# Kernel tuning notes

Measured on AMD Instinct MI355X. Metric: run time of the kernel, lower is better.

The kernel has to match this reference:

```python
import jax, jax.numpy as jnp
import numpy as np

N_NODES = 50000
N_EDGES = 800000
D_IN, D1, D2, D_OUT = 128, 150, 100, 64


def setup_inputs() -> dict:
    key = jax.random.key(0)
    ks = jax.random.split(key, 10)
    x = jax.random.normal(ks[0], (N_NODES, D_IN), dtype=jnp.float32)
    src = jax.random.randint(ks[1], (N_EDGES,), 0, N_NODES, dtype=jnp.int32)
    dst = jax.random.randint(ks[2], (N_EDGES,), 0, N_NODES, dtype=jnp.int32)
    s1 = 1.0 / np.sqrt(D_IN)
    s2 = 1.0 / np.sqrt(D1)
    s3 = 1.0 / np.sqrt(D2)
    W1 = jax.random.uniform(ks[3], (D_IN, D1), jnp.float32, -s1, s1)
    b1 = jnp.zeros((D1,), jnp.float32)
    Wn = jax.random.uniform(ks[4], (D1, D2), jnp.float32, -s2, s2)
    Ws = jax.random.uniform(ks[5], (D1, D2), jnp.float32, -s2, s2)
    b2 = jnp.zeros((D2,), jnp.float32)
    W3 = jax.random.uniform(ks[6], (D2, D_OUT), jnp.float32, -s3, s3)
    b3 = jnp.zeros((D_OUT,), jnp.float32)
    return {"x": x, "src": src, "dst": dst, "W1": W1, "b1": b1,
            "Wn": Wn, "Ws": Ws, "b2": b2, "W3": W3, "b3": b3}


def _degrees(src, dst, n):
    ones = jnp.ones(src.shape[0], jnp.float32)
    deg_out = jax.ops.segment_sum(ones, src, num_segments=n)
    deg_in = jax.ops.segment_sum(ones, dst, num_segments=n)
    return deg_out, deg_in


def reference(x, src, dst, W1, b1, Wn, Ws, b2, W3, b3):
    n = x.shape[0]
    deg_out, deg_in = _degrees(src, dst, n)
    norm_out = jax.lax.rsqrt(jnp.maximum(deg_out, 1.0))  # [N]
    norm_in = jax.lax.rsqrt(jnp.maximum(deg_in, 1.0))    # [N]

    # --- GraphConv (norm='both'): D_in^{-1/2} A D_out^{-1/2} X W + b ---
    h = x * norm_out[:, None]                                   # [N, D_IN]
    agg = jax.ops.segment_sum(h[src], dst, num_segments=n)      # [N, D_IN]
    h = (agg * norm_in[:, None]) @ W1 + b1                      # [N, D1]
    h = jax.nn.elu(h)

    # --- SAGEConv (mean): fc_self(h) + fc_neigh(mean_neighbors(h)) + b ---
    neigh_sum = jax.ops.segment_sum(h[src], dst, num_segments=n)  # [N, D1]
    neigh = neigh_sum / jnp.maximum(deg_in, 1.0)[:, None]
    h = h @ Ws + neigh @ Wn + b2                                  # [N, D2]
    h = jax.nn.elu(h)

    # --- Dense + ELU ---
    out = jax.nn.elu(h @ W3 + b3)                                 # [N, D_OUT]
    return out
```

## Files before the change

kernel.cpp:

```cpp
#include <hip/hip_runtime.h>
#include <math.h>

#define N_NODES 50000
#define N_EDGES 800000
#define D_IN 128
#define D1 150
#define LD1 152
#define D2 100
#define LDP 100
#define D_OUT 64
#define SLOT 64
#define HBLK 64
#define HBIN 12500

#define LDS_K 40

using short8 = __attribute__((ext_vector_type(8))) short;
using f32x4  = __attribute__((ext_vector_type(4))) float;

__device__ __forceinline__ float elu(float v) { return v > 0.0f ? v : expm1f(v); }

__device__ __forceinline__ void split_bf16(float a, unsigned short& h, unsigned short& l) {
    unsigned int bits = __float_as_uint(a);
    unsigned int hb = (bits + 0x8000u) >> 16;
    h = (unsigned short)hb;
    float r = a - __uint_as_float(hb << 16);
    l = (unsigned short)((__float_as_uint(r) + 0x8000u) >> 16);
}

__device__ __forceinline__ void split8(const float4 a, const float4 b, short8& h, short8& l) {
    float f[8] = {a.x, a.y, a.z, a.w, b.x, b.y, b.z, b.w};
#pragma unroll
    for (int i = 0; i < 8; ++i) {
        unsigned short hh, ll;
        split_bf16(f[i], hh, ll);
        h[i] = (short)hh; l[i] = (short)ll;
    }
}

__device__ __forceinline__ float4 g_load4(const float* p) { return *(const float4*)p; }

__device__ __forceinline__ float4 g_load4_guard(const float* row, int kbase, int Klim, bool rowok) {
    float4 v;
    v.x = (rowok && kbase + 0 < Klim) ? row[kbase + 0] : 0.0f;
    v.y = (rowok && kbase + 1 < Klim) ? row[kbase + 1] : 0.0f;
    v.z = (rowok && kbase + 2 < Klim) ? row[kbase + 2] : 0.0f;
    v.w = (rowok && kbase + 3 < Klim) ? row[kbase + 3] : 0.0f;
    return v;
}

__device__ __forceinline__ void barrier_lgkm() {
    asm volatile("s_waitcnt lgkmcnt(0)\n\ts_barrier" ::: "memory");
    __builtin_amdgcn_sched_barrier(0);
}

__global__ __launch_bounds__(256) void hist_kernel(const int* __restrict__ src,
                                                   unsigned int* __restrict__ partial) {
    __shared__ unsigned int bins[HBIN];
    int tid = threadIdx.x, b = blockIdx.x;
    for (int i = tid; i < HBIN; i += 256) bins[i] = 0u;
    __syncthreads();
    int e0 = b * (N_EDGES / HBLK);
    int e1 = e0 + (N_EDGES / HBLK);
    for (int e = e0 + tid; e < e1; e += 256) {
        int s = src[e];
        atomicAdd(&bins[s >> 2], 1u << ((s & 3) * 8));
    }
    __syncthreads();
    unsigned int* outp = partial + (size_t)b * HBIN;
    for (int i = tid; i < HBIN; i += 256) outp[i] = bins[i];
}

__global__ __launch_bounds__(256) void norm_kernel(const unsigned int* __restrict__ partial,
                                                   float* __restrict__ norm_out) {
    int i = blockIdx.x * blockDim.x + threadIdx.x;
    if (i >= HBIN) return;
    unsigned int acc = 0;
#pragma unroll
    for (int h = 0; h < HBLK; ++h) acc += partial[(size_t)h * HBIN + i];
#pragma unroll
    for (int j = 0; j < 4; ++j) {
        unsigned int dg = (acc >> (j * 8)) & 0xFF;
        norm_out[i * 4 + j] = rsqrtf(fmaxf((float)dg, 1.0f));
    }
}

__global__ void fill_kernel(const int* __restrict__ src, const int* __restrict__ dst,
                            int* __restrict__ cursor, unsigned short* __restrict__ slots) {
    int e = blockIdx.x * blockDim.x + threadIdx.x;
    if (e < N_EDGES) {
        int d = dst[e], s = src[e];
        int pos = atomicAdd(&cursor[d], 1);
        if (pos < SLOT) slots[d * SLOT + pos] = (unsigned short)s;
    }
}

__global__ __launch_bounds__(256) void gather_x(const float* __restrict__ x,
                                                const float* __restrict__ norm_out,
                                                const int* __restrict__ deg_in,
                                                const unsigned short* __restrict__ slots,
                                                float* __restrict__ agg) {
    int wave = threadIdx.x >> 6;
    int lane = threadIdx.x & 63;
    int half = lane >> 5;
    int c = lane & 31;
    int n = blockIdx.x * 4 + wave;
    if (n >= N_NODES) return;
    int beg = n * SLOT;
    int dg = deg_in[n]; if (dg > SLOT) dg = SLOT;
    int end = beg + dg;
    float4 acc = {0.0f, 0.0f, 0.0f, 0.0f};
    int e = beg + half;
    for (; e + 6 < end; e += 8) {
        int s0 = slots[e];
        int s1 = slots[e + 2];
        int s2 = slots[e + 4];
        int s3 = slots[e + 6];
        float w0 = norm_out[s0], w1 = norm_out[s1];
        float w2 = norm_out[s2], w3 = norm_out[s3];
        float4 v0 = ((const float4*)(x + (size_t)s0 * D_IN))[c];
        float4 v1 = ((const float4*)(x + (size_t)s1 * D_IN))[c];
        float4 v2 = ((const float4*)(x + (size_t)s2 * D_IN))[c];
        float4 v3 = ((const float4*)(x + (size_t)s3 * D_IN))[c];
        acc.x += v0.x * w0 + v1.x * w1 + v2.x * w2 + v3.x * w3;
        acc.y += v0.y * w0 + v1.y * w1 + v2.y * w2 + v3.y * w3;
        acc.z += v0.z * w0 + v1.z * w1 + v2.z * w2 + v3.z * w3;
        acc.w += v0.w * w0 + v1.w * w1 + v2.w * w2 + v3.w * w3;
    }
    for (; e < end; e += 2) {
        int s = slots[e];
        float w = norm_out[s];
        float4 v = ((const float4*)(x + (size_t)s * D_IN))[c];
        acc.x += v.x * w; acc.y += v.y * w; acc.z += v.z * w; acc.w += v.w * w;
    }
    acc.x += __shfl_xor(acc.x, 32);
    acc.y += __shfl_xor(acc.y, 32);
    acc.z += __shfl_xor(acc.z, 32);
    acc.w += __shfl_xor(acc.w, 32);
    if (half == 0) ((float4*)(agg + (size_t)n * D_IN))[c] = acc;
}

__global__ __launch_bounds__(256) void gather_p(const float* __restrict__ p,
                                                const int* __restrict__ deg_in,
                                                const unsigned short* __restrict__ slots,
                                                float* __restrict__ ns) {
    int wave = threadIdx.x >> 6;
    int lane = threadIdx.x & 63;
    int half = lane >> 5;
    int c = lane & 31;
    bool cv = c < D2 / 4;
    int n = blockIdx.x * 4 + wave;
    if (n >= N_NODES) return;
    int beg = n * SLOT;
    int dg = deg_in[n]; if (dg > SLOT) dg = SLOT;
    int end = beg + dg;
    float4 acc = {0.0f, 0.0f, 0.0f, 0.0f};
    if (cv) {
        int e = beg + half;
        for (; e + 6 < end; e += 8) {
            int s0 = slots[e];
            int s1 = slots[e + 2];
            int s2 = slots[e + 4];
            int s3 = slots[e + 6];
            float4 v0 = ((const float4*)(p + (size_t)s0 * LDP))[c];
            float4 v1 = ((const float4*)(p + (size_t)s1 * LDP))[c];
            float4 v2 = ((const float4*)(p + (size_t)s2 * LDP))[c];
            float4 v3 = ((const float4*)(p + (size_t)s3 * LDP))[c];
            acc.x += (v0.x + v1.x) + (v2.x + v3.x);
            acc.y += (v0.y + v1.y) + (v2.y + v3.y);
            acc.z += (v0.z + v1.z) + (v2.z + v3.z);
            acc.w += (v0.w + v1.w) + (v2.w + v3.w);
        }
        for (; e < end; e += 2) {
            int s = slots[e];
            float4 v = ((const float4*)(p + (size_t)s * LDP))[c];
            acc.x += v.x; acc.y += v.y; acc.z += v.z; acc.w += v.w;
        }
    }
    acc.x += __shfl_xor(acc.x, 32);
    acc.y += __shfl_xor(acc.y, 32);
    acc.z += __shfl_xor(acc.z, 32);
    acc.w += __shfl_xor(acc.w, 32);
    if (half == 0 && cv) ((float4*)(ns + (size_t)n * LDP))[c] = acc;
}

template <int K, int KP, int NW, int LDA, int PRE, int EPI, int LDC, int GROUP>
__global__ __launch_bounds__(256, 5)
void gemm_mfma(const float* __restrict__ A, const float* __restrict__ W,
               const float* __restrict__ nsrc, const int* __restrict__ deg,
               const float* __restrict__ bstage, const float* __restrict__ bepi,
               float* __restrict__ C) {
    constexpr int NSTEP = KP / 32;
    constexpr int MBLK = (N_NODES + 63) / 64;
    __shared__ __align__(16) unsigned short AsH[64][LDS_K];
    __shared__ __align__(16) unsigned short AsL[64][LDS_K];
    __shared__ __align__(16) unsigned short BsH[64][LDS_K];
    __shared__ __align__(16) unsigned short BsL[64][LDS_K];

    const int b = blockIdx.x;
    const int cxcd = b & 7;
    const int sIdx = b >> 3;
    const int jj = sIdx / GROUP;
    const int yy = sIdx - jj * GROUP;
    const int xb = cxcd + 8 * jj;
    if (xb >= MBLK) return;
    const int m0 = xb * 64;
    const int n0 = yy * 64;

    const int tid = threadIdx.x;
    const int arow = tid >> 2;
    const int ak = (tid & 3) * 8;
    const int grow = m0 + arow;
    const bool rowok = grow < N_NODES;
    const int bn = tid & 63;
    const int bkg = tid >> 6;
    const int bcol = n0 + bn;
    const int wid = tid >> 6;
    const int lane = tid & 63;
    const int wm = (wid >> 1) * 32;
    const int wn = (wid & 1) * 32;
    const int fr = lane & 15;
    const int fg = lane >> 4;

    float invd = 1.0f;
    if (PRE) {
        int dv = rowok ? deg[grow] : 1;
        invd = 1.0f / fmaxf((float)dv, 1.0f);
    }

    f32x4 acc[2][2];
#pragma unroll
    for (int i = 0; i < 2; ++i)
#pragma unroll
        for (int j = 0; j < 2; ++j) acc[i][j] = {0.0f, 0.0f, 0.0f, 0.0f};

    const float* arp = A + (size_t)grow * LDA;
    const float* nrp = PRE ? (nsrc + (size_t)grow * LDP) : nullptr;

    float4 pa[2][2], pn[2][2];
    float pb[2][8];

    {
        if (rowok && 32 <= K) {
            pa[0][0] = g_load4(arp + ak);
            pa[0][1] = g_load4(arp + ak + 4);
        } else {
            pa[0][0] = g_load4_guard(arp, ak, K, rowok);
            pa[0][1] = g_load4_guard(arp, ak + 4, K, rowok);
        }
        if (PRE) {
            if (rowok && 32 <= K) {
                pn[0][0] = g_load4(nrp + ak);
                pn[0][1] = g_load4(nrp + ak + 4);
            } else {
                pn[0][0] = g_load4_guard(nrp, ak, K, rowok);
                pn[0][1] = g_load4_guard(nrp, ak + 4, K, rowok);
            }
        }
#pragma unroll
        for (int kk = 0; kk < 8; ++kk) {
            int k = bkg * 8 + kk;
            pb[0][kk] = (k < K && bcol < NW) ? W[(size_t)k * NW + bcol] : 0.0f;
        }
    }

#pragma unroll
    for (int t = 0; t < NSTEP; ++t) {
        const int cur = t & 1, nxt = cur ^ 1;
        if (t + 1 < NSTEP) {
            const int k0n = (t + 1) * 32;
            if (rowok && k0n + 32 <= K) {
                pa[nxt][0] = g_load4(arp + k0n + ak);
                pa[nxt][1] = g_load4(arp + k0n + ak + 4);
            } else {
                pa[nxt][0] = g_load4_guard(arp, k0n + ak, K, rowok);
                pa[nxt][1] = g_load4_guard(arp, k0n + ak + 4, K, rowok);
            }
            if (PRE) {
                if (rowok && k0n + 32 <= K) {
                    pn[nxt][0] = g_load4(nrp + k0n + ak);
                    pn[nxt][1] = g_load4(nrp + k0n + ak + 4);
                } else {
                    pn[nxt][0] = g_load4_guard(nrp, k0n + ak, K, rowok);
                    pn[nxt][1] = g_load4_guard(nrp, k0n + ak + 4, K, rowok);
                }
            }
#pragma unroll
            for (int kk = 0; kk < 8; ++kk) {
                int k = k0n + bkg * 8 + kk;
                pb[nxt][kk] = (k < K && bcol < NW) ? W[(size_t)k * NW + bcol] : 0.0f;
            }
        }
        barrier_lgkm();
        {
            const int k0 = t * 32;
            float4 va0 = pa[cur][0], va1 = pa[cur][1];
            if (PRE) {
                const float4 vn0 = pn[cur][0], vn1 = pn[cur][1];
                if (k0 + 32 <= K) {
                    va0.x = elu(va0.x + bstage[k0 + ak + 0] + vn0.x * invd);
                    va0.y = elu(va0.y + bstage[k0 + ak + 1] + vn0.y * invd);
                    va0.z = elu(va0.z + bstage[k0 + ak + 2] + vn0.z * invd);
                    va0.w = elu(va0.w + bstage[k0 + ak + 3] + vn0.w * invd);
                    va1.x = elu(va1.x + bstage[k0 + ak + 4] + vn1.x * invd);
                    va1.y = elu(va1.y + bstage[k0 + ak + 5] + vn1.y * invd);
                    va1.z = elu(va1.z + bstage[k0 + ak + 6] + vn1.z * invd);
                    va1.w = elu(va1.w + bstage[k0 + ak + 7] + vn1.w * invd);
                } else {
                    va0.x = (k0 + ak + 0 < K) ? elu(va0.x + bstage[k0 + ak + 0] + vn0.x * invd) : 0.0f;
                    va0.y = (k0 + ak + 1 < K) ? elu(va0.y + bstage[k0 + ak + 1] + vn0.y * invd) : 0.0f;
                    va0.z = (k0 + ak + 2 < K) ? elu(va0.z + bstage[k0 + ak + 2] + vn0.z * invd) : 0.0f;
                    va0.w = (k0 + ak + 3 < K) ? elu(va0.w + bstage[k0 + ak + 3] + vn0.w * invd) : 0.0f;
                    va1.x = (k0 + ak + 4 < K) ? elu(va1.x + bstage[k0 + ak + 4] + vn1.x * invd) : 0.0f;
                    va1.y = (k0 + ak + 5 < K) ? elu(va1.y + bstage[k0 + ak + 5] + vn1.y * invd) : 0.0f;
                    va1.z = (k0 + ak + 6 < K) ? elu(va1.z + bstage[k0 + ak + 6] + vn1.z * invd) : 0.0f;
                    va1.w = (k0 + ak + 7 < K) ? elu(va1.w + bstage[k0 + ak + 7] + vn1.w * invd) : 0.0f;
                }
            }
            short8 h8, l8;
            split8(va0, va1, h8, l8);
            *(short8*)&AsH[arow][ak] = h8;
            *(short8*)&AsL[arow][ak] = l8;
            float4 vb0, vb1;
            vb0.x = pb[cur][0]; vb0.y = pb[cur][1]; vb0.z = pb[cur][2]; vb0.w = pb[cur][3];
            vb1.x = pb[cur][4]; vb1.y = pb[cur][5]; vb1.z = pb[cur][6]; vb1.w = pb[cur][7];
            split8(vb0, vb1, h8, l8);
            *(short8*)&BsH[bn][bkg * 8] = h8;
            *(short8*)&BsL[bn][bkg * 8] = l8;
        }
        barrier_lgkm();
        {
            short8 ah0 = *(const short8*)&AsH[wm + fr][fg * 8];
            short8 ah1 = *(const short8*)&AsH[wm + 16 + fr][fg * 8];
            short8 al0 = *(const short8*)&AsL[wm + fr][fg * 8];
            short8 al1 = *(const short8*)&AsL[wm + 16 + fr][fg * 8];
            short8 bh0 = *(const short8*)&BsH[wn + fr][fg * 8];
            short8 bh1 = *(const short8*)&BsH[wn + 16 + fr][fg * 8];
            short8 bl0 = *(const short8*)&BsL[wn + fr][fg * 8];
            short8 bl1 = *(const short8*)&BsL[wn + 16 + fr][fg * 8];
            acc[0][0] = __builtin_amdgcn_mfma_f32_16x16x32_bf16(ah0, bh0, acc[0][0], 0, 0, 0);
            acc[0][0] = __builtin_amdgcn_mfma_f32_16x16x32_bf16(al0, bh0, acc[0][0], 0, 0, 0);
            acc[0][0] = __builtin_amdgcn_mfma_f32_16x16x32_bf16(ah0, bl0, acc[0][0], 0, 0, 0);
            acc[0][1] = __builtin_amdgcn_mfma_f32_16x16x32_bf16(ah0, bh1, acc[0][1], 0, 0, 0);
            acc[0][1] = __builtin_amdgcn_mfma_f32_16x16x32_bf16(al0, bh1, acc[0][1], 0, 0, 0);
            acc[0][1] = __builtin_amdgcn_mfma_f32_16x16x32_bf16(ah0, bl1, acc[0][1], 0, 0, 0);
            acc[1][0] = __builtin_amdgcn_mfma_f32_16x16x32_bf16(ah1, bh0, acc[1][0], 0, 0, 0);
            acc[1][0] = __builtin_amdgcn_mfma_f32_16x16x32_bf16(al1, bh0, acc[1][0], 0, 0, 0);
            acc[1][0] = __builtin_amdgcn_mfma_f32_16x16x32_bf16(ah1, bl0, acc[1][0], 0, 0, 0);
            acc[1][1] = __builtin_amdgcn_mfma_f32_16x16x32_bf16(ah1, bh1, acc[1][1], 0, 0, 0);
            acc[1][1] = __builtin_amdgcn_mfma_f32_16x16x32_bf16(al1, bh1, acc[1][1], 0, 0, 0);
            acc[1][1] = __builtin_amdgcn_mfma_f32_16x16x32_bf16(ah1, bl1, acc[1][1], 0, 0, 0);
        }
    }

#pragma unroll
    for (int fi = 0; fi < 2; ++fi) {
#pragma unroll
        for (int r = 0; r < 4; ++r) {
            int row = m0 + wm + fi * 16 + fg * 4 + r;
            if (row >= N_NODES) continue;
            float rmul = 1.0f;
            if (EPI == 1) rmul = rsqrtf(fmaxf((float)deg[row], 1.0f));
#pragma unroll
            for (int fj = 0; fj < 2; ++fj) {
                int col = n0 + wn + fj * 16 + fr;
                if (col >= LDC) continue;
                float v = 0.0f;
                if (col < NW) {
                    v = acc[fi][fj][r];
                    if (EPI == 1) v = elu(v * rmul + bepi[col]);
                    else if (EPI == 3) v = elu(v + bepi[col]);
                }
                C[(size_t)row * LDC + col] = v;
            }
        }
    }
}

__global__ __launch_bounds__(256, 5)
void gemm_dual_mfma(const float* __restrict__ h1, const float* __restrict__ Wn,
                    const float* __restrict__ Ws, float* __restrict__ p,
                    float* __restrict__ h2pre) {
    constexpr int NSTEP = 5;
    constexpr int MBLK = (N_NODES + 63) / 64;
    __shared__ __align__(16) unsigned short AsH[64][LDS_K];
    __shared__ __align__(16) unsigned short AsL[64][LDS_K];
    __shared__ __align__(16) unsigned short BsH[64][LDS_K];
    __shared__ __align__(16) unsigned short BsL[64][LDS_K];

    const int b = blockIdx.x;
    const int cxcd = b & 7;
    const int sIdx = b >> 3;
    const int jj = sIdx >> 2;
    const int yy = sIdx & 3;
    const int xb = cxcd + 8 * jj;
    if (xb >= MBLK) return;
    const int m0 = xb * 64;
    const int n0 = (yy & 1) * 64;
    const float* W = (yy < 2) ? Wn : Ws;

    const int tid = threadIdx.x;
    const int arow = tid >> 2;
    const int ak = (tid & 3) * 8;
    const int grow = m0 + arow;
    const bool rowok = grow < N_NODES;
    const int bn = tid & 63;
    const int bkg = tid >> 6;
    const int bcol = n0 + bn;
    const int wid = tid >> 6;
    const int lane = tid & 63;
    const int wm = (wid >> 1) * 32;
    const int wn = (wid & 1) * 32;
    const int fr = lane & 15;
    const int fg = lane >> 4;

    f32x4 acc[2][2];
#pragma unroll
    for (int i = 0; i < 2; ++i)
#pragma unroll
        for (int j = 0; j < 2; ++j) acc[i][j] = {0.0f, 0.0f, 0.0f, 0.0f};

    const float* arp = h1 + (size_t)grow * LD1;

    float4 pa[2][2];
    float pb[2][8];

    {
        if (rowok) {
            pa[0][0] = g_load4(arp + ak);
            pa[0][1] = g_load4(arp + ak + 4);
        } else {
            pa[0][0] = g_load4_guard(arp, ak, D1, rowok);
            pa[0][1] = g_load4_guard(arp, ak + 4, D1, rowok);
        }
#pragma unroll
        for (int kk = 0; kk < 8; ++kk) {
            int k = bkg * 8 + kk;
            pb[0][kk] = (k < D1 && bcol < D2) ? W[(size_t)k * D2 + bcol] : 0.0f;
        }
    }

#pragma unroll
    for (int t = 0; t < NSTEP; ++t) {
        const int cur = t & 1, nxt = cur ^ 1;
        if (t + 1 < NSTEP) {
            const int k0n = (t + 1) * 32;
            if (rowok && k0n + 32 <= D1) {
                pa[nxt][0] = g_load4(arp + k0n + ak);
                pa[nxt][1] = g_load4(arp + k0n + ak + 4);
            } else {
                pa[nxt][0] = g_load4_guard(arp, k0n + ak, D1, rowok);
                pa[nxt][1] = g_load4_guard(arp, k0n + ak + 4, D1, rowok);
            }
#pragma unroll
            for (int kk = 0; kk < 8; ++kk) {
                int k = k0n + bkg * 8 + kk;
                pb[nxt][kk] = (k < D1 && bcol < D2) ? W[(size_t)k * D2 + bcol] : 0.0f;
            }
        }
        barrier_lgkm();
        {
            short8 h8, l8;
            split8(pa[cur][0], pa[cur][1], h8, l8);
            *(short8*)&AsH[arow][ak] = h8;
            *(short8*)&AsL[arow][ak] = l8;
            float4 vb0, vb1;
            vb0.x = pb[cur][0]; vb0.y = pb[cur][1]; vb0.z = pb[cur][2]; vb0.w = pb[cur][3];
            vb1.x = pb[cur][4]; vb1.y = pb[cur][5]; vb1.z = pb[cur][6]; vb1.w = pb[cur][7];
            split8(vb0, vb1, h8, l8);
            *(short8*)&BsH[bn][bkg * 8] = h8;
            *(short8*)&BsL[bn][bkg * 8] = l8;
        }
        barrier_lgkm();
        {
            short8 ah0 = *(const short8*)&AsH[wm + fr][fg * 8];
            short8 ah1 = *(const short8*)&AsH[wm + 16 + fr][fg * 8];
            short8 al0 = *(const short8*)&AsL[wm + fr][fg * 8];
            short8 al1 = *(const short8*)&AsL[wm + 16 + fr][fg * 8];
            short8 bh0 = *(const short8*)&BsH[wn + fr][fg * 8];
            short8 bh1 = *(const short8*)&BsH[wn + 16 + fr][fg * 8];
            short8 bl0 = *(const short8*)&BsL[wn + fr][fg * 8];
            short8 bl1 = *(const short8*)&BsL[wn + 16 + fr][fg * 8];
            acc[0][0] = __builtin_amdgcn_mfma_f32_16x16x32_bf16(ah0, bh0, acc[0][0], 0, 0, 0);
            acc[0][0] = __builtin_amdgcn_mfma_f32_16x16x32_bf16(al0, bh0, acc[0][0], 0, 0, 0);
            acc[0][0] = __builtin_amdgcn_mfma_f32_16x16x32_bf16(ah0, bl0, acc[0][0], 0, 0, 0);
            acc[0][1] = __builtin_amdgcn_mfma_f32_16x16x32_bf16(ah0, bh1, acc[0][1], 0, 0, 0);
            acc[0][1] = __builtin_amdgcn_mfma_f32_16x16x32_bf16(al0, bh1, acc[0][1], 0, 0, 0);
            acc[0][1] = __builtin_amdgcn_mfma_f32_16x16x32_bf16(ah0, bl1, acc[0][1], 0, 0, 0);
            acc[1][0] = __builtin_amdgcn_mfma_f32_16x16x32_bf16(ah1, bh0, acc[1][0], 0, 0, 0);
            acc[1][0] = __builtin_amdgcn_mfma_f32_16x16x32_bf16(al1, bh0, acc[1][0], 0, 0, 0);
            acc[1][0] = __builtin_amdgcn_mfma_f32_16x16x32_bf16(ah1, bl0, acc[1][0], 0, 0, 0);
            acc[1][1] = __builtin_amdgcn_mfma_f32_16x16x32_bf16(ah1, bh1, acc[1][1], 0, 0, 0);
            acc[1][1] = __builtin_amdgcn_mfma_f32_16x16x32_bf16(al1, bh1, acc[1][1], 0, 0, 0);
            acc[1][1] = __builtin_amdgcn_mfma_f32_16x16x32_bf16(ah1, bl1, acc[1][1], 0, 0, 0);
        }
    }

#pragma unroll
    for (int fi = 0; fi < 2; ++fi) {
#pragma unroll
        for (int r = 0; r < 4; ++r) {
            int row = m0 + wm + fi * 16 + fg * 4 + r;
            if (row >= N_NODES) continue;
#pragma unroll
            for (int fj = 0; fj < 2; ++fj) {
                int col = n0 + wn + fj * 16 + fr;
                float v = acc[fi][fj][r];
                if (col < D2) {
                    if (yy < 2) p[(size_t)row * LDP + col] = v;
                    else        h2pre[(size_t)row * D2 + col] = v;
                }
            }
        }
    }
}

extern "C" void kernel_launch(void* const* d_in, const int* in_sizes, int n_in,
                              void* d_out, int out_size, void* d_ws, size_t ws_size,
                              hipStream_t stream) {
    const float* x  = (const float*)d_in[0];
    const int* src  = (const int*)d_in[1];
    const int* dst  = (const int*)d_in[2];
    const float* W1 = (const float*)d_in[3];
    const float* b1 = (const float*)d_in[4];
    const float* Wn = (const float*)d_in[5];
    const float* Ws = (const float*)d_in[6];
    const float* b2 = (const float*)d_in[7];
    const float* W3 = (const float*)d_in[8];
    const float* b3 = (const float*)d_in[9];
    float* out = (float*)d_out;

    char* wsb = (char*)d_ws;
    unsigned int* partial = (unsigned int*)wsb;
    int*   cursor     = (int*)wsb + 800000;
    float* norm_out   = (float*)wsb + 850000;
    unsigned short* slots = (unsigned short*)((float*)wsb + 900000);
    float* agg        = (float*)wsb + 2500000;
    float* h1         = (float*)wsb + 8900000;
    float* h2pre      = (float*)wsb + 16500000;
    float* p          = agg;
    float* ns         = h1;
    int*   deg_in     = cursor;

    hipMemsetAsync(cursor, 0, N_NODES * sizeof(int), stream);

    hist_kernel<<<HBLK, 256, 0, stream>>>(src, partial);
    fill_kernel<<<(N_EDGES + 255) / 256, 256, 0, stream>>>(src, dst, cursor, slots);
    norm_kernel<<<(HBIN + 255) / 256, 256, 0, stream>>>(partial, norm_out);
    gather_x<<<(N_NODES + 3) / 4, 256, 0, stream>>>(x, norm_out, deg_in, slots, agg);

    const int MB = (N_NODES + 63) / 64;
    const int XG = (MB + 7) / 8;
    gemm_mfma<128, 128, 150, 128, 0, 1, LD1, 3><<<XG * 8 * 3, 256, 0, stream>>>(
        agg, W1, nullptr, deg_in, nullptr, b1, h1);
    gemm_dual_mfma<<<XG * 8 * 4, 256, 0, stream>>>(h1, Wn, Ws, p, h2pre);
    gather_p<<<(N_NODES + 3) / 4, 256, 0, stream>>>(p, deg_in, slots, ns);
    gemm_mfma<100, 128, 64, 100, 1, 3, D_OUT, 1><<<XG * 8, 256, 0, stream>>>(
        h2pre, W3, ns, deg_in, b2, b3, out);
}
```

Measured before the change: 335.0 us.

## Partition gather_x feature columns across XCDs for L2 locality

Restructures the x-gather so each block handles only a 32-column chunk of the 128 features. Block indices are mapped so that each pair of XCDs owns one column chunk, with lanes split as 8 edges by 8 float4 columns. The goal is for each XCD's L2 to cache a quarter of x rather than all of it, cutting L2 misses on the random neighbor reads. In exchange it launches four times as many blocks, reads slots and norm_out four times over, adds extra shuffle reductions, and removes the 4-way unrolled loop.

```diff
diff --git a/kernel.cpp b/kernel.cpp
--- a/kernel.cpp
+++ b/kernel.cpp
@@ -100,44 +100,36 @@
                                                 const int* __restrict__ deg_in,
                                                 const unsigned short* __restrict__ slots,
                                                 float* __restrict__ agg) {
+    int b = blockIdx.x;
+    int xcd = b & 7;
+    int chunk = xcd >> 1;
+    int sub = xcd & 1;
+    int slot = b >> 3;
+    int nb = slot * 2 + sub;
     int wave = threadIdx.x >> 6;
     int lane = threadIdx.x & 63;
-    int half = lane >> 5;
-    int c = lane & 31;
-    int n = blockIdx.x * 4 + wave;
+    int eslot = lane >> 3;
+    int c = lane & 7;
+    int n = nb * 4 + wave;
     if (n >= N_NODES) return;
     int beg = n * SLOT;
     int dg = deg_in[n]; if (dg > SLOT) dg = SLOT;
     int end = beg + dg;
+    int cbase = chunk * 8;
     float4 acc = {0.0f, 0.0f, 0.0f, 0.0f};
-    int e = beg + half;
-    for (; e + 6 < end; e += 8) {
-        int s0 = slots[e];
-        int s1 = slots[e + 2];
-        int s2 = slots[e + 4];
-        int s3 = slots[e + 6];
-        float w0 = norm_out[s0], w1 = norm_out[s1];
-        float w2 = norm_out[s2], w3 = norm_out[s3];
-        float4 v0 = ((const float4*)(x + (size_t)s0 * D_IN))[c];
-        float4 v1 = ((const float4*)(x + (size_t)s1 * D_IN))[c];
-        float4 v2 = ((const float4*)(x + (size_t)s2 * D_IN))[c];
-        float4 v3 = ((const float4*)(x + (size_t)s3 * D_IN))[c];
-        acc.x += v0.x * w0 + v1.x * w1 + v2.x * w2 + v3.x * w3;
-        acc.y += v0.y * w0 + v1.y * w1 + v2.y * w2 + v3.y * w3;
-        acc.z += v0.z * w0 + v1.z * w1 + v2.z * w2 + v3.z * w3;
-        acc.w += v0.w * w0 + v1.w * w1 + v2.w * w2 + v3.w * w3;
-    }
-    for (; e < end; e += 2) {
+    for (int e = beg + eslot; e < end; e += 8) {
         int s = slots[e];
         float w = norm_out[s];
-        float4 v = ((const float4*)(x + (size_t)s * D_IN))[c];
+        float4 v = ((const float4*)(x + (size_t)s * D_IN))[cbase + c];
         acc.x += v.x * w; acc.y += v.y * w; acc.z += v.z * w; acc.w += v.w * w;
     }
-    acc.x += __shfl_xor(acc.x, 32);
-    acc.y += __shfl_xor(acc.y, 32);
-    acc.z += __shfl_xor(acc.z, 32);
-    acc.w += __shfl_xor(acc.w, 32);
-    if (half == 0) ((float4*)(agg + (size_t)n * D_IN))[c] = acc;
+    acc.x += __shfl_xor(acc.x, 8);  acc.y += __shfl_xor(acc.y, 8);
+    acc.z += __shfl_xor(acc.z, 8);  acc.w += __shfl_xor(acc.w, 8);
+    acc.x += __shfl_xor(acc.x, 16); acc.y += __shfl_xor(acc.y, 16);
+    acc.z += __shfl_xor(acc.z, 16); acc.w += __shfl_xor(acc.w, 16);
+    acc.x += __shfl_xor(acc.x, 32); acc.y += __shfl_xor(acc.y, 32);
+    acc.z += __shfl_xor(acc.z, 32); acc.w += __shfl_xor(acc.w, 32);
+    if (eslot == 0) ((float4*)(agg + (size_t)n * D_IN))[cbase + c] = acc;
 }
 
 __global__ __launch_bounds__(256) void gather_p(const float* __restrict__ p,
@@ -547,7 +539,7 @@
     hist_kernel<<<HBLK, 256, 0, stream>>>(src, partial);
     fill_kernel<<<(N_EDGES + 255) / 256, 256, 0, stream>>>(src, dst, cursor, slots);
     norm_kernel<<<(HBIN + 255) / 256, 256, 0, stream>>>(partial, norm_out);
-    gather_x<<<(N_NODES + 3) / 4, 256, 0, stream>>>(x, norm_out, deg_in, slots, agg);
+    gather_x<<<6250 * 8, 256, 0, stream>>>(x, norm_out, deg_in, slots, agg);
 
     const int MB = (N_NODES + 63) / 64;
     const int XG = (MB + 7) / 8;
```

After: 349.1 us. +4.2%, slower.
